# Optimization experiments

Hardware: AMD Instinct MI355X
Metric: run time of the kernel (lower is better)

Reference implementation:

```python
import jax, jax.numpy as jnp
import numpy as np

N_NODES = 131072
N_EDGES = 2097152
B = 256
NODES_PER_GRAPH = 512  # uniform graphs -> to_dense_batch == reshape
F_IN = 74
D = 128
L = 3
EPS = 1e-5


def setup_inputs() -> dict:
    key = jax.random.key(0)
    ks = jax.random.split(key, 12)
    x = jax.random.normal(ks[0], (N_NODES, F_IN), dtype=jnp.float32)
    edge_index = jax.random.randint(ks[1], (2, N_EDGES), 0, N_NODES, dtype=jnp.int32)
    batch = (jnp.arange(N_NODES, dtype=jnp.int32) // NODES_PER_GRAPH)
    s = 1.0 / np.sqrt(D)
    W_init = jax.random.uniform(ks[2], (F_IN, D), jnp.float32, -s, s)
    W_gcn = jax.random.uniform(ks[3], (L, D, D), jnp.float32, -s, s)
    b_gcn = jnp.zeros((L, D), jnp.float32)
    gamma = jnp.ones((L, D), jnp.float32)
    beta = jnp.zeros((L, D), jnp.float32)
    W_res = jax.random.uniform(ks[4], (L, D, D), jnp.float32, -s, s)
    b_res = jax.random.uniform(ks[5], (L, D), jnp.float32, -s, s)
    return {"x": x, "edge_index": edge_index, "batch": batch, "W_init": W_init,
            "W_gcn": W_gcn, "b_gcn": b_gcn, "gamma": gamma, "beta": beta,
            "W_res": W_res, "b_res": b_res}


def _gcn_conv(x, src, tgt, norm, W, b):
    # PyG GCNConv: h = x @ W ; out[tgt] += norm * h[src] ; + bias
    h = x @ W                                    # [N, D]
    msg = h[src] * norm[:, None]                 # [E+N, D] gather (memory-bound)
    out = jax.ops.segment_sum(msg, tgt, num_segments=N_NODES)
    return out + b


def _batchnorm(x, g, bta):
    mean = jnp.mean(x, axis=0)
    var = jnp.var(x, axis=0)  # biased, matches torch BN training forward
    return (x - mean) * jax.lax.rsqrt(var + EPS) * g + bta


def reference(x, edge_index, batch, W_init, W_gcn, b_gcn, gamma, beta, W_res, b_res):
    # add self loops once; symmetric deg^{-1/2} normalization (PyG default)
    loops = jnp.arange(N_NODES, dtype=edge_index.dtype)
    src = jnp.concatenate([edge_index[0], loops])
    tgt = jnp.concatenate([edge_index[1], loops])
    deg = jax.ops.segment_sum(jnp.ones_like(src, dtype=jnp.float32), tgt,
                              num_segments=N_NODES)
    dinv = jnp.where(deg > 0, jax.lax.rsqrt(jnp.maximum(deg, 1.0)), 0.0)
    norm = dinv[src] * dinv[tgt]

    h = x @ W_init                               # init_transform (no bias)
    for i in range(L):
        conv = _gcn_conv(h, src, tgt, norm, W_gcn[i], b_gcn[i])
        h_new = jax.nn.relu(_batchnorm(conv, gamma[i], beta[i]))
        h = h_new + (h @ W_res[i] + b_res[i])
    # to_dense_batch with uniform NODES_PER_GRAPH -> reshape, all mask=True
    return h.reshape(B, NODES_PER_GRAPH, D)
```

## Files before the change

kernel.cpp:

```cpp
#include <hip/hip_runtime.h>

#define NN 131072
#define NE 2097152
#define DD 128
#define LL 3

#define NB 256
#define BSH 9
#define TILE (NE / NB)

typedef __attribute__((ext_vector_type(8))) short short8;
typedef __attribute__((ext_vector_type(4))) float f32x4;

__device__ __forceinline__ ushort f2bf(float f) {
    uint u = __float_as_uint(f);
    return (ushort)((u + 0x7fffu + ((u >> 16) & 1u)) >> 16);
}
__device__ __forceinline__ float bflo(uint u) { return __uint_as_float(u << 16); }
__device__ __forceinline__ float bfhi(uint u) { return __uint_as_float(u & 0xffff0000u); }

__global__ __launch_bounds__(256) void k_prep(const float* __restrict__ x,
                                              const float* __restrict__ Wi,
                                              const float* __restrict__ Wg,
                                              const float* __restrict__ Wr,
                                              uint* __restrict__ xb,
                                              ushort* __restrict__ wt,
                                              float* __restrict__ bns) {
    const int t = threadIdx.x, blk = blockIdx.x;
    const size_t id = (size_t)blk * 256 + t;
    const int n = (int)(id >> 6);
    const int k0 = (int)(id & 63) * 2;
    float v0 = (k0 < 74) ? x[(size_t)n * 74 + k0] : 0.0f;
    float v1 = (k0 + 1 < 74) ? x[(size_t)n * 74 + k0 + 1] : 0.0f;
    xb[id] = (uint)f2bf(v0) | ((uint)f2bf(v1) << 16);
    if (blk < 448) {
        const int id2 = blk * 256 + t;
        const int m = id2 >> 14;
        const int c = (id2 >> 7) & 127;
        const int k = id2 & 127;
        float v;
        if (m == 0)      v = (k < 74) ? Wi[k * DD + c] : 0.0f;
        else if (m <= 3) v = Wg[(size_t)(m - 1) * DD * DD + k * DD + c];
        else             v = Wr[(size_t)(m - 4) * DD * DD + k * DD + c];
        wt[id2] = f2bf(v);
    }
    if (blk == 448) {
        bns[t] = 0.0f; bns[t + 256] = 0.0f; bns[t + 512] = 0.0f;
    }
}

__global__ __launch_bounds__(256) void kA_count(const int* __restrict__ tgt,
                                                int* __restrict__ blockHist) {
    __shared__ int hist[NB];
    const int t = threadIdx.x, blk = blockIdx.x;
    hist[t] = 0;
    __syncthreads();
    const int base = blk * TILE;
#pragma unroll 8
    for (int j = 0; j < TILE / 256; ++j)
        atomicAdd(&hist[tgt[base + j * 256 + t] >> BSH], 1);
    __syncthreads();
    blockHist[t * NB + blk] = hist[t];
}

__global__ __launch_bounds__(256) void kA_scan1(int* __restrict__ blockHist,
                                                int* __restrict__ rowSum) {
    __shared__ int sc[256];
    const int t = threadIdx.x, b = blockIdx.x;
    const int v = blockHist[b * NB + t];
    sc[t] = v;
    __syncthreads();
    for (int off = 1; off < 256; off <<= 1) {
        int a = sc[t];
        int u = (t >= off) ? sc[t - off] : 0;
        __syncthreads();
        sc[t] = a + u;
        __syncthreads();
    }
    blockHist[b * NB + t] = sc[t] - v;
    if (t == 255) rowSum[b] = sc[255];
}

__global__ __launch_bounds__(256) void kA_scan2(const int* __restrict__ rowSum,
                                                int* __restrict__ bstart) {
    __shared__ int sc[256];
    const int t = threadIdx.x;
    const int v = rowSum[t];
    sc[t] = v;
    __syncthreads();
    for (int off = 1; off < 256; off <<= 1) {
        int a = sc[t];
        int u = (t >= off) ? sc[t - off] : 0;
        __syncthreads();
        sc[t] = a + u;
        __syncthreads();
    }
    bstart[t] = sc[t] - v;
    if (t == 255) bstart[NB] = sc[255];
}

__global__ __launch_bounds__(256) void kA_scatter(const int* __restrict__ src,
                                                  const int* __restrict__ tgt,
                                                  const int* __restrict__ chunkBase,
                                                  const int* __restrict__ bstart,
                                                  uint* __restrict__ packed) {
    __shared__ int cur[NB];
    const int t = threadIdx.x, blk = blockIdx.x;
    cur[t] = bstart[t] + chunkBase[t * NB + blk];
    __syncthreads();
    const int base = blk * TILE;
#pragma unroll 4
    for (int j = 0; j < TILE / 256; ++j) {
        const int e = base + j * 256 + t;
        const int tg = tgt[e], s = src[e];
        const int b = tg >> BSH;
        const int pos = atomicAdd(&cur[b], 1);
        packed[pos] = (uint)s | ((uint)(tg & ((1 << BSH) - 1)) << 17);
    }
}

__global__ __launch_bounds__(256) void kB_sort(const uint* __restrict__ packed,
                                               const int* __restrict__ bstart,
                                               int* __restrict__ rowp,
                                               float* __restrict__ dinv,
                                               int* __restrict__ deg,
                                               int* __restrict__ ssrc) {
    __shared__ int cnt[1 << BSH];
    __shared__ int pscan[256];
    const int t = threadIdx.x, b = blockIdx.x;
    const int e0 = bstart[b], e1 = bstart[b + 1];
    cnt[t] = 0; cnt[t + 256] = 0;
    __syncthreads();
    for (int e = e0 + t; e < e1; e += 256)
        atomicAdd(&cnt[packed[e] >> 17], 1);
    __syncthreads();
    const int c0 = cnt[2 * t], c1 = cnt[2 * t + 1];
    pscan[t] = c0 + c1;
    __syncthreads();
    for (int off = 1; off < 256; off <<= 1) {
        int v = pscan[t];
        int u = (t >= off) ? pscan[t - off] : 0;
        __syncthreads();
        pscan[t] = v + u;
        __syncthreads();
    }
    const int ex0 = pscan[t] - c0 - c1;
    const int ex1 = ex0 + c0;
    const int n0 = (b << BSH) + 2 * t;
    rowp[n0] = e0 + ex0;
    rowp[n0 + 1] = e0 + ex1;
    dinv[n0] = rsqrtf((float)(c0 + 1));
    dinv[n0 + 1] = rsqrtf((float)(c1 + 1));
    deg[n0] = c0 + 1;
    deg[n0 + 1] = c1 + 1;
    if (b == NB - 1 && t == 255) rowp[NN] = e1;
    __syncthreads();
    cnt[2 * t] = ex0;
    cnt[2 * t + 1] = ex1;
    __syncthreads();
    for (int e = e0 + t; e < e1; e += 256) {
        const uint p = packed[e];
        const int tl = p >> 17;
        const int pos = atomicAdd(&cnt[tl], 1);
        ssrc[e0 + pos] = (int)(p & 0x1FFFFu);
    }
}

__global__ __launch_bounds__(256) void k_pack(int* __restrict__ ssrc,
                                              const int* __restrict__ deg) {
    const int e = blockIdx.x * 256 + threadIdx.x;
    const int s = ssrc[e];
    ssrc[e] = s | (deg[s] << 17);
}

template <int MODE>
__global__ __launch_bounds__(256) void k_mgemm(const ushort* A,
                                               const ushort* __restrict__ Bt,
                                               ushort* outb,
                                               float* __restrict__ outf,
                                               const ushort* __restrict__ convb,
                                               const float* __restrict__ gamma,
                                               const float* __restrict__ beta,
                                               const float* __restrict__ bres,
                                               float* __restrict__ bnsums) {
    __shared__ ushort As[16384];
    __shared__ ushort Bs[16384];
    __shared__ float sred[256];
    const int t = threadIdx.x;
    const int w = t >> 6, l = t & 63;
    const int lc = l & 15, lr = l >> 4;
    const size_t row0 = (size_t)blockIdx.x * 128;

    for (int ch = w * 8; ch < w * 8 + 8; ++ch) {
        const int row = ch * 4 + lr;
        const int kb = (lc * 16) ^ ((row & 7) << 4);
        const ushort* srcA = A + (row0 + row) * DD + (kb >> 1);
        const ushort* srcB = Bt + (size_t)row * DD + (kb >> 1);
        __builtin_amdgcn_global_load_lds(
            (const __attribute__((address_space(1))) void*)srcA,
            (__attribute__((address_space(3))) void*)(As + ch * 512), 16, 0, 0);
        __builtin_amdgcn_global_load_lds(
            (const __attribute__((address_space(1))) void*)srcB,
            (__attribute__((address_space(3))) void*)(Bs + ch * 512), 16, 0, 0);
    }
    if (MODE == 1) sred[t] = 0.0f;
    if (MODE >= 2 && t < DD) {
        const float invN = 1.0f / (float)NN;
        const float mean = bnsums[t] * invN;
        const float var = bnsums[DD + t] * invN - mean * mean;
        const float sc = gamma[t] * rsqrtf(var + 1e-5f);
        sred[t] = sc;
        sred[DD + t] = beta[t] - mean * sc;
    }
    __syncthreads();

    f32x4 acc[2][8] = {};
    const char* Ab = (const char*)As;
    const char* Bb = (const char*)Bs;
#pragma unroll
    for (int kk = 0; kk < 4; ++kk) {
        const int kb = kk * 64 + lr * 16;
        short8 a[2];
#pragma unroll
        for (int m = 0; m < 2; ++m) {
            const int r = w * 32 + m * 16 + lc;
            a[m] = *(const short8*)(Ab + r * 256 + (kb ^ ((r & 7) << 4)));
        }
#pragma unroll
        for (int n = 0; n < 8; ++n) {
            const int c = n * 16 + lc;
            short8 b = *(const short8*)(Bb + c * 256 + (kb ^ ((c & 7) << 4)));
            acc[0][n] = __builtin_amdgcn_mfma_f32_16x16x32_bf16(a[0], b, acc[0][n], 0, 0, 0);
            acc[1][n] = __builtin_amdgcn_mfma_f32_16x16x32_bf16(a[1], b, acc[1][n], 0, 0, 0);
        }
    }

    if (MODE == 0) {
#pragma unroll
        for (int m = 0; m < 2; ++m)
#pragma unroll
            for (int n = 0; n < 8; ++n) {
                const int c = n * 16 + lc;
#pragma unroll
                for (int j = 0; j < 4; ++j) {
                    const size_t r = row0 + w * 32 + m * 16 + lr * 4 + j;
                    outb[r * DD + c] = f2bf(acc[m][n][j]);
                }
            }
    } else if (MODE == 1) {
#pragma unroll
        for (int n = 0; n < 8; ++n) {
            const int c = n * 16 + lc;
            float ps = 0.0f, ps2 = 0.0f;
#pragma unroll
            for (int m = 0; m < 2; ++m)
#pragma unroll
                for (int j = 0; j < 4; ++j) {
                    const size_t r = row0 + w * 32 + m * 16 + lr * 4 + j;
                    const float v = acc[m][n][j];
                    outb[r * DD + c] = f2bf(v);
                    ps += v; ps2 += v * v;
                }
            atomicAdd(&sred[c], ps);
            atomicAdd(&sred[DD + c], ps2);
        }
        __syncthreads();
        atomicAdd(&bnsums[t], sred[t]);
    } else {
        float scv[8], shv[8], bbv[8];
#pragma unroll
        for (int n = 0; n < 8; ++n) {
            const int c = n * 16 + lc;
            scv[n] = sred[c]; shv[n] = sred[DD + c]; bbv[n] = bres[c];
        }
#pragma unroll
        for (int m = 0; m < 2; ++m)
#pragma unroll
            for (int n = 0; n < 8; ++n) {
                const int c = n * 16 + lc;
#pragma unroll
                for (int j = 0; j < 4; ++j) {
                    const size_t r = row0 + w * 32 + m * 16 + lr * 4 + j;
                    const float cv = __uint_as_float((uint)convb[r * DD + c] << 16);
                    const float v = fmaxf(cv * scv[n] + shv[n], 0.0f) + acc[m][n][j] + bbv[n];
                    if (MODE == 2) outb[r * DD + c] = f2bf(v);
                    if (MODE == 3) outf[r * DD + c] = v;
                }
            }
    }
}

__global__ __launch_bounds__(256) void k_aggregate(const int* __restrict__ rowp,
                                                   const float* __restrict__ dinv,
                                                   const int* __restrict__ ssrc,
                                                   const uint* __restrict__ hb,
                                                   uint* __restrict__ aggb) {
    const int n = blockIdx.x * 4 + (threadIdx.x >> 6);
    const int l = threadIdx.x & 63;
    const float dn = dinv[n];
    const uint u0 = hb[((uint)n << 6) + l];
    const float dn2 = dn * dn;
    float ax = dn2 * bflo(u0), ay = dn2 * bfhi(u0);
    const int e0 = rowp[n], e1 = rowp[n + 1];
    for (int base = e0; base < e1; base += 64) {
        const int cnt = min(64, e1 - base);
        int sv = 0; float nm = 0.0f;
        if (l < cnt) {
            const uint p = (uint)ssrc[base + l];
            sv = (int)(p & 0x1FFFFu);
            nm = dn * rsqrtf((float)(p >> 17));
        }
        int i = 0;
        for (; i + 16 <= cnt; i += 16) {
            uint vv[16]; float nmv[16];
#pragma unroll
            for (int j = 0; j < 16; ++j) {
                const int s = __shfl(sv, i + j);
                nmv[j] = __shfl(nm, i + j);
                vv[j] = hb[((uint)s << 6) + l];
            }
#pragma unroll
            for (int j = 0; j < 16; ++j) {
                ax += nmv[j] * bflo(vv[j]);
                ay += nmv[j] * bfhi(vv[j]);
            }
        }
        for (; i < cnt; i += 8) {
            uint vv[8]; float nmv[8];
#pragma unroll
            for (int j = 0; j < 8; ++j) {
                const int s = __shfl(sv, i + j);
                nmv[j] = __shfl(nm, i + j);
                vv[j] = hb[((uint)s << 6) + l];
            }
#pragma unroll
            for (int j = 0; j < 8; ++j) {
                ax += nmv[j] * bflo(vv[j]);
                ay += nmv[j] * bfhi(vv[j]);
            }
        }
    }
    aggb[((uint)n << 6) + l] = (uint)f2bf(ax) | ((uint)f2bf(ay) << 16);
}

extern "C" void kernel_launch(void* const* d_in, const int* in_sizes, int n_in,
                              void* d_out, int out_size, void* d_ws, size_t ws_size,
                              hipStream_t stream) {
    const float* x      = (const float*)d_in[0];
    const int*   ei     = (const int*)d_in[1];
    const float* W_init = (const float*)d_in[3];
    const float* W_gcn  = (const float*)d_in[4];
    const float* gamma  = (const float*)d_in[6];
    const float* beta   = (const float*)d_in[7];
    const float* W_res  = (const float*)d_in[8];
    const float* b_res  = (const float*)d_in[9];

    float* h = (float*)d_out;
    char* p = (char*)d_ws;
    ushort* aggb = (ushort*)p;           p += (size_t)NN * DD * 2;
    ushort* hb   = (ushort*)p;           p += (size_t)NN * DD * 2;
    ushort* convb = (ushort*)p;          p += (size_t)NN * DD * 2;
    uint*   xb   = (uint*)convb;
    float*  dinv = (float*)p;            p += (size_t)NN * 4;
    int*    deg  = (int*)p;              p += (size_t)NN * 4;
    float*  bns  = (float*)p;            p += 768 * 4;
    ushort* wt   = (ushort*)p;           p += 7 * 16384 * 2;
    int* blockHist = (int*)p;            p += (size_t)NB * NB * 4;
    int* rowSum  = (int*)p;              p += NB * 4;
    int* bstart  = (int*)p;              p += (NB + 1) * 4 + 4;
    uint* packed = (uint*)p;             p += (size_t)NE * 4;
    int* rowp    = (int*)p;              p += ((size_t)NN + 1) * 4 + 4;
    int* ssrc    = (int*)p;

    const int* srcp = ei;
    const int* tgtp = ei + NE;

    k_prep<<<NN * 64 / 256, 256, 0, stream>>>(x, W_init, W_gcn, W_res, xb, wt, bns);
    kA_count<<<NB, 256, 0, stream>>>(tgtp, blockHist);
    kA_scan1<<<NB, 256, 0, stream>>>(blockHist, rowSum);
    kA_scan2<<<1, 256, 0, stream>>>(rowSum, bstart);
    kA_scatter<<<NB, 256, 0, stream>>>(srcp, tgtp, blockHist, bstart, packed);
    kB_sort<<<NB, 256, 0, stream>>>(packed, bstart, rowp, dinv, deg, ssrc);
    k_pack<<<NE / 256, 256, 0, stream>>>(ssrc, deg);

    k_mgemm<0><<<NN / 128, 256, 0, stream>>>((const ushort*)xb, wt, hb,
                                             nullptr, nullptr, nullptr, nullptr,
                                             nullptr, nullptr);

    for (int i = 0; i < LL; ++i) {
        k_aggregate<<<NN / 4, 256, 0, stream>>>(rowp, dinv, ssrc,
                                                (const uint*)hb, (uint*)aggb);
        k_mgemm<1><<<NN / 128, 256, 0, stream>>>(aggb, wt + (size_t)(1 + i) * 16384,
                                                 convb, nullptr, nullptr, nullptr,
                                                 nullptr, nullptr, bns + i * 256);
        if (i < LL - 1)
            k_mgemm<2><<<NN / 128, 256, 0, stream>>>(hb, wt + (size_t)(4 + i) * 16384,
                                                     hb, nullptr, convb,
                                                     gamma + i * DD, beta + i * DD,
                                                     b_res + i * DD, bns + i * 256);
        else
            k_mgemm<3><<<NN / 128, 256, 0, stream>>>(hb, wt + (size_t)(4 + i) * 16384,
                                                     nullptr, h, convb,
                                                     gamma + i * DD, beta + i * DD,
                                                     b_res + i * DD, bns + i * 256);
    }
}
```

Before: 533.5 us.

## Use 8-wave GEMM blocks and LDS-staged edge lists in aggregation

The dense GEMM kernel now runs with 512 threads (8 waves), each wave computing a 16-row slab instead of 32 rows, which halves accumulator registers per wave and spreads the LDS load work over more waves. The aggregation kernel stages each 64-edge chunk's (norm, pre-shifted source offset) pairs in shared memory and reads them back with broadcast LDS loads, replacing the two cross-lane shuffles per edge. This trades more threads per GEMM block and extra LDS traffic for lower register pressure and cheaper per-edge index and weight fetches.

```diff
diff --git a/kernel.cpp b/kernel.cpp
--- a/kernel.cpp
+++ b/kernel.cpp
@@ -174,7 +174,7 @@
 }
 
 template <int MODE>
-__global__ __launch_bounds__(256) void k_mgemm(const ushort* A,
+__global__ __launch_bounds__(512) void k_mgemm(const ushort* A,
                                                const ushort* __restrict__ Bt,
                                                ushort* outb,
                                                float* __restrict__ outf,
@@ -191,7 +191,7 @@
     const int lc = l & 15, lr = l >> 4;
     const size_t row0 = (size_t)blockIdx.x * 128;
 
-    for (int ch = w * 8; ch < w * 8 + 8; ++ch) {
+    for (int ch = w * 4; ch < w * 4 + 4; ++ch) {
         const int row = ch * 4 + lr;
         const int kb = (lc * 16) ^ ((row & 7) << 4);
         const ushort* srcA = A + (row0 + row) * DD + (kb >> 1);
@@ -203,7 +203,7 @@
             (const __attribute__((address_space(1))) void*)srcB,
             (__attribute__((address_space(3))) void*)(Bs + ch * 512), 16, 0, 0);
     }
-    if (MODE == 1) sred[t] = 0.0f;
+    if (MODE == 1 && t < 256) sred[t] = 0.0f;
     if (MODE >= 2 && t < DD) {
         const float invN = 1.0f / (float)NN;
         const float mean = bnsums[t] * invN;
@@ -214,58 +214,49 @@
     }
     __syncthreads();
 
-    f32x4 acc[2][8] = {};
+    f32x4 acc[8] = {};
     const char* Ab = (const char*)As;
     const char* Bb = (const char*)Bs;
 #pragma unroll
     for (int kk = 0; kk < 4; ++kk) {
         const int kb = kk * 64 + lr * 16;
-        short8 a[2];
-#pragma unroll
-        for (int m = 0; m < 2; ++m) {
-            const int r = w * 32 + m * 16 + lc;
-            a[m] = *(const short8*)(Ab + r * 256 + (kb ^ ((r & 7) << 4)));
-        }
+        const int r = w * 16 + lc;
+        const short8 a = *(const short8*)(Ab + r * 256 + (kb ^ ((r & 7) << 4)));
 #pragma unroll
         for (int n = 0; n < 8; ++n) {
             const int c = n * 16 + lc;
             short8 b = *(const short8*)(Bb + c * 256 + (kb ^ ((c & 7) << 4)));
-            acc[0][n] = __builtin_amdgcn_mfma_f32_16x16x32_bf16(a[0], b, acc[0][n], 0, 0, 0);
-            acc[1][n] = __builtin_amdgcn_mfma_f32_16x16x32_bf16(a[1], b, acc[1][n], 0, 0, 0);
+            acc[n] = __builtin_amdgcn_mfma_f32_16x16x32_bf16(a, b, acc[n], 0, 0, 0);
         }
     }
 
     if (MODE == 0) {
 #pragma unroll
-        for (int m = 0; m < 2; ++m)
-#pragma unroll
-            for (int n = 0; n < 8; ++n) {
-                const int c = n * 16 + lc;
-#pragma unroll
-                for (int j = 0; j < 4; ++j) {
-                    const size_t r = row0 + w * 32 + m * 16 + lr * 4 + j;
-                    outb[r * DD + c] = f2bf(acc[m][n][j]);
-                }
-            }
+        for (int n = 0; n < 8; ++n) {
+            const int c = n * 16 + lc;
+#pragma unroll
+            for (int j = 0; j < 4; ++j) {
+                const size_t r = row0 + w * 16 + lr * 4 + j;
+                outb[r * DD + c] = f2bf(acc[n][j]);
+            }
+        }
     } else if (MODE == 1) {
 #pragma unroll
         for (int n = 0; n < 8; ++n) {
             const int c = n * 16 + lc;
             float ps = 0.0f, ps2 = 0.0f;
 #pragma unroll
-            for (int m = 0; m < 2; ++m)
-#pragma unroll
-                for (int j = 0; j < 4; ++j) {
-                    const size_t r = row0 + w * 32 + m * 16 + lr * 4 + j;
-                    const float v = acc[m][n][j];
-                    outb[r * DD + c] = f2bf(v);
-                    ps += v; ps2 += v * v;
-                }
+            for (int j = 0; j < 4; ++j) {
+                const size_t r = row0 + w * 16 + lr * 4 + j;
+                const float v = acc[n][j];
+                outb[r * DD + c] = f2bf(v);
+                ps += v; ps2 += v * v;
+            }
             atomicAdd(&sred[c], ps);
             atomicAdd(&sred[DD + c], ps2);
         }
         __syncthreads();
-        atomicAdd(&bnsums[t], sred[t]);
+        if (t < 256) atomicAdd(&bnsums[t], sred[t]);
     } else {
         float scv[8], shv[8], bbv[8];
 #pragma unroll
@@ -274,19 +265,17 @@
             scv[n] = sred[c]; shv[n] = sred[DD + c]; bbv[n] = bres[c];
         }
 #pragma unroll
-        for (int m = 0; m < 2; ++m)
-#pragma unroll
-            for (int n = 0; n < 8; ++n) {
-                const int c = n * 16 + lc;
-#pragma unroll
-                for (int j = 0; j < 4; ++j) {
-                    const size_t r = row0 + w * 32 + m * 16 + lr * 4 + j;
-                    const float cv = __uint_as_float((uint)convb[r * DD + c] << 16);
-                    const float v = fmaxf(cv * scv[n] + shv[n], 0.0f) + acc[m][n][j] + bbv[n];
-                    if (MODE == 2) outb[r * DD + c] = f2bf(v);
-                    if (MODE == 3) outf[r * DD + c] = v;
-                }
-            }
+        for (int n = 0; n < 8; ++n) {
+            const int c = n * 16 + lc;
+#pragma unroll
+            for (int j = 0; j < 4; ++j) {
+                const size_t r = row0 + w * 16 + lr * 4 + j;
+                const float cv = __uint_as_float((uint)convb[r * DD + c] << 16);
+                const float v = fmaxf(cv * scv[n] + shv[n], 0.0f) + acc[n][j] + bbv[n];
+                if (MODE == 2) outb[r * DD + c] = f2bf(v);
+                if (MODE == 3) outf[r * DD + c] = v;
+            }
+        }
     }
 }
 
@@ -295,7 +284,9 @@
                                                    const int* __restrict__ ssrc,
                                                    const uint* __restrict__ hb,
                                                    uint* __restrict__ aggb) {
-    const int n = blockIdx.x * 4 + (threadIdx.x >> 6);
+    __shared__ float2 eb[4][64];
+    const int wv = threadIdx.x >> 6;
+    const int n = blockIdx.x * 4 + wv;
     const int l = threadIdx.x & 63;
     const float dn = dinv[n];
     const uint u0 = hb[((uint)n << 6) + l];
@@ -304,20 +295,21 @@
     const int e0 = rowp[n], e1 = rowp[n + 1];
     for (int base = e0; base < e1; base += 64) {
         const int cnt = min(64, e1 - base);
-        int sv = 0; float nm = 0.0f;
+        float nm = 0.0f; uint sb = 0;
         if (l < cnt) {
             const uint p = (uint)ssrc[base + l];
-            sv = (int)(p & 0x1FFFFu);
+            sb = (p & 0x1FFFFu) << 6;
             nm = dn * rsqrtf((float)(p >> 17));
         }
+        eb[wv][l] = make_float2(nm, __uint_as_float(sb));
         int i = 0;
         for (; i + 16 <= cnt; i += 16) {
             uint vv[16]; float nmv[16];
 #pragma unroll
             for (int j = 0; j < 16; ++j) {
-                const int s = __shfl(sv, i + j);
-                nmv[j] = __shfl(nm, i + j);
-                vv[j] = hb[((uint)s << 6) + l];
+                const float2 e = eb[wv][i + j];
+                nmv[j] = e.x;
+                vv[j] = hb[__float_as_uint(e.y) + l];
             }
 #pragma unroll
             for (int j = 0; j < 16; ++j) {
@@ -329,9 +321,9 @@
             uint vv[8]; float nmv[8];
 #pragma unroll
             for (int j = 0; j < 8; ++j) {
-                const int s = __shfl(sv, i + j);
-                nmv[j] = __shfl(nm, i + j);
-                vv[j] = hb[((uint)s << 6) + l];
+                const float2 e = eb[wv][i + j];
+                nmv[j] = e.x;
+                vv[j] = hb[__float_as_uint(e.y) + l];
             }
 #pragma unroll
             for (int j = 0; j < 8; ++j) {
@@ -383,23 +375,23 @@
     kB_sort<<<NB, 256, 0, stream>>>(packed, bstart, rowp, dinv, deg, ssrc);
     k_pack<<<NE / 256, 256, 0, stream>>>(ssrc, deg);
 
-    k_mgemm<0><<<NN / 128, 256, 0, stream>>>((const ushort*)xb, wt, hb,
+    k_mgemm<0><<<NN / 128, 512, 0, stream>>>((const ushort*)xb, wt, hb,
                                              nullptr, nullptr, nullptr, nullptr,
                                              nullptr, nullptr);
 
     for (int i = 0; i < LL; ++i) {
         k_aggregate<<<NN / 4, 256, 0, stream>>>(rowp, dinv, ssrc,
                                                 (const uint*)hb, (uint*)aggb);
-        k_mgemm<1><<<NN / 128, 256, 0, stream>>>(aggb, wt + (size_t)(1 + i) * 16384,
+        k_mgemm<1><<<NN / 128, 512, 0, stream>>>(aggb, wt + (size_t)(1 + i) * 16384,
                                                  convb, nullptr, nullptr, nullptr,
                                                  nullptr, nullptr, bns + i * 256);
         if (i < LL - 1)
-            k_mgemm<2><<<NN / 128, 256, 0, stream>>>(hb, wt + (size_t)(4 + i) * 16384,
+            k_mgemm<2><<<NN / 128, 512, 0, stream>>>(hb, wt + (size_t)(4 + i) * 16384,
                                                      hb, nullptr, convb,
                                                      gamma + i * DD, beta + i * DD,
                                                      b_res + i * DD, bns + i * 256);
         else
-            k_mgemm<3><<<NN / 128, 256, 0, stream>>>(hb, wt + (size_t)(4 + i) * 16384,
+            k_mgemm<3><<<NN / 128, 512, 0, stream>>>(hb, wt + (size_t)(4 + i) * 16384,
                                                      nullptr, h, convb,
                                                      gamma + i * DD, beta + i * DD,
                                                      b_res + i * DD, bns + i * 256);
```

After: 550.8 us. +3.2%, slower.
